# Optimization experiments

Hardware: AMD Instinct MI355X
Metric: run time of the kernel (lower is better)

## Reference

```python
import jax, jax.numpy as jnp
import numpy as np

BOHR_RADIUS = 0.529177  # Angstrom
KE_KCAL = 332.0636      # Coulomb constant, kcal/mol * Angstrom / e^2
EPS = 1e-15
R_CUT = 5.0

ZBL = {'d': [0.8854 * BOHR_RADIUS], 'z_exp': [0.23],
       'c': [0.1818, 0.5099, 0.2802, 0.02817],
       'exponents': [3.2, 0.9423, 0.4028, 0.2016]}

def _inv_softplus(v):
    v = np.asarray(v, dtype=np.float32)
    return jnp.asarray(np.log(np.exp(v) - 1.0).reshape(-1, 1))

def setup_inputs() -> dict:
    key = jax.random.key(0)
    k1, k2, k3, k4 = jax.random.split(key, 4)
    N, E, M = 200000, 8000000, 1000
    xyz = jax.random.normal(k1, (N, 3), dtype=jnp.float32) * 3.0
    z = jax.random.randint(k2, (N,), 1, 94, dtype=jnp.int32)
    nbrs = jax.random.randint(k3, (E, 2), 0, N, dtype=jnp.int32)
    offsets = jax.random.normal(k4, (E, 3), dtype=jnp.float32) * 2.0
    num_atoms = jnp.full((M,), N // M, dtype=jnp.int32)
    return {
        'xyz': xyz, 'z': z, 'nbrs': nbrs, 'num_atoms': num_atoms, 'offsets': offsets,
        'd_inv': _inv_softplus(ZBL['d']),
        'z_exp_inv': _inv_softplus(ZBL['z_exp']),
        'c_inv': _inv_softplus(ZBL['c']),
        'exponents_inv': _inv_softplus(ZBL['exponents']),
    }

def reference(xyz, z, nbrs, num_atoms, offsets, d_inv, z_exp_inv, c_inv, exponents_inv):
    sp = jax.nn.softplus
    d, z_exp, c, exponents = sp(d_inv), sp(z_exp_inv), sp(c_inv), sp(exponents_inv)

    i, j = nbrs[:, 0], nbrs[:, 1]
    mask = j > i  # undirected-edge filter (masked instead of gathered: same math)

    z_i = z[i].astype(jnp.float32)  # [E]
    z_j = z[j].astype(jnp.float32)
    diff = xyz[i] - xyz[j] - offsets                  # [E,3]
    r_ij = jnp.sqrt((diff ** 2 + EPS).sum(-1))        # stable norm, [E]

    # ZBL phi: d,z_exp are [1,1]; broadcast over edges
    a = (d / (z_i ** z_exp + z_j ** z_exp)).reshape(-1)           # [E]
    phi = (c * jnp.exp(-exponents * r_ij / a)).sum(0) / c.sum()   # [4,E] -> [E]

    # SpookyNet cutoff, NaN-safe outside r_cut
    den = (R_CUT - r_ij) * (R_CUT + r_ij)
    safe_den = jnp.where(r_ij < R_CUT, den, 1.0)
    f_cut = jnp.where(r_ij < R_CUT, jnp.exp(-r_ij ** 2 / safe_den), 0.0)

    pairwise = KE_KCAL * z_i * z_j / r_ij * phi * f_cut
    pairwise = jnp.where(mask, pairwise, 0.0)

    N = xyz.shape[0]
    M = num_atoms.shape[0]
    mol_idx = jnp.repeat(jnp.arange(M), num_atoms, total_repeat_length=N)  # [N]
    seg = mol_idx[i]                                                       # [E]
    energy = jax.ops.segment_sum(pairwise, seg, num_segments=M).reshape(-1, 1)
    return energy
```

## Files before the change

kernel.cpp:

```cpp
#include <hip/hip_runtime.h>
#include <hip/hip_bf16.h>

#define KE_F  332.0636f
#define MAX_M 1024
#define BLK   256
#define NBLK  2048

typedef int   ivec4 __attribute__((ext_vector_type(4)));
typedef float fvec4 __attribute__((ext_vector_type(4)));

__device__ __forceinline__ float softplusf(float x) {
    return logf(1.0f + expf(x));
}

__global__ void scan_params_kernel(const int* __restrict__ num_atoms, int M,
                                   const float* __restrict__ d_inv,
                                   const float* __restrict__ z_exp_inv,
                                   const float* __restrict__ c_inv,
                                   const float* __restrict__ exp_inv,
                                   int* __restrict__ mol_starts,
                                   float* __restrict__ params,
                                   float* __restrict__ out) {
    __shared__ int buf[MAX_M];
    int t = threadIdx.x;
    buf[t] = (t < M) ? num_atoms[t] : 0;
    __syncthreads();
    for (int off = 1; off < MAX_M; off <<= 1) {
        int x = (t >= off) ? buf[t - off] : 0;
        __syncthreads();
        buf[t] += x;
        __syncthreads();
    }
    if (t == 0) mol_starts[0] = 0;
    if (t < M) mol_starts[t + 1] = buf[t];
    if (t == 0) {
        float dd = softplusf(d_inv[0]);
        float c0 = softplusf(c_inv[0]), c1 = softplusf(c_inv[1]);
        float c2 = softplusf(c_inv[2]), c3 = softplusf(c_inv[3]);
        float e0 = softplusf(exp_inv[0]), e1 = softplusf(exp_inv[1]);
        float e2 = softplusf(exp_inv[2]), e3 = softplusf(exp_inv[3]);
        float ic = 1.0f / (c0 + c1 + c2 + c3);
        float id = 1.0f / dd;
        params[0] = c0 * ic; params[1] = c1 * ic; params[2] = c2 * ic; params[3] = c3 * ic;
        params[4] = e0 * id; params[5] = e1 * id; params[6] = e2 * id; params[7] = e3 * id;
    }
    if (t < 96) {
        float zexp = softplusf(z_exp_inv[0]);
        params[16 + t] = __powf((float)t, zexp);
    }
    for (int k = t; k < M; k += MAX_M) out[k] = 0.0f;
}

__global__ void pack_kernel(const float* __restrict__ xyz,
                            const int* __restrict__ z,
                            const int* __restrict__ mol_starts, int M, int N,
                            float4* __restrict__ pack) {
    int a = blockIdx.x * blockDim.x + threadIdx.x;
    if (a >= N) return;
    int lo = 0, hi = M;
    while (hi - lo > 1) {
        int mid = (lo + hi) >> 1;
        if (mol_starts[mid] <= a) lo = mid; else hi = mid;
    }
    pack[a] = make_float4(xyz[3 * a + 0], xyz[3 * a + 1], xyz[3 * a + 2],
                          (float)((lo << 7) | z[a]));
}

__global__ __launch_bounds__(BLK) void nr_main_kernel(
    const int* __restrict__ nbrs, const float* __restrict__ offsets,
    const float4* __restrict__ pack,
    const float* __restrict__ params, float* __restrict__ out, int E, int M) {
    __shared__ float sm[MAX_M];
    __shared__ float zp[96];
    for (int t = threadIdx.x; t < MAX_M; t += BLK) sm[t] = 0.0f;
    if (threadIdx.x < 96) zp[threadIdx.x] = params[16 + threadIdx.x];
    __syncthreads();

    const float4 kk = *(const float4*)(params + 0);
    const float4 gg = *(const float4*)(params + 4);

    const int ngroups = E >> 2;
    const int stride = gridDim.x * BLK;
    const ivec4* nb4 = (const ivec4*)nbrs;
    const fvec4* of4 = (const fvec4*)offsets;

    for (int g = blockIdx.x * BLK + threadIdx.x; g < ngroups; g += stride) {
        const ivec4 n01 = __builtin_nontemporal_load(nb4 + 2 * (size_t)g);
        const ivec4 n23 = __builtin_nontemporal_load(nb4 + 2 * (size_t)g + 1);
        const fvec4 oA  = __builtin_nontemporal_load(of4 + 3 * (size_t)g);
        const fvec4 oB  = __builtin_nontemporal_load(of4 + 3 * (size_t)g + 1);
        const fvec4 oC  = __builtin_nontemporal_load(of4 + 3 * (size_t)g + 2);

        const int   iv[4] = {n01.x, n01.z, n23.x, n23.z};
        const int   jv[4] = {n01.y, n01.w, n23.y, n23.w};
        const float ox[4] = {oA.x, oA.w, oB.z, oC.y};
        const float oy[4] = {oA.y, oB.x, oB.w, oC.z};
        const float oz[4] = {oA.z, oB.y, oC.x, oC.w};

        bool   m[4];
        float4 pi[4], pj[4];
#pragma unroll
        for (int k = 0; k < 4; ++k) {
            m[k] = jv[k] > iv[k];
            const int ii = m[k] ? iv[k] : 0;
            const int jj = m[k] ? jv[k] : 0;
            pi[k] = pack[ii];
            pj[k] = pack[jj];
        }
#pragma unroll
        for (int k = 0; k < 4; ++k) {
            const float dx = pi[k].x - pj[k].x - ox[k];
            const float dy = pi[k].y - pj[k].y - oy[k];
            const float dz = pi[k].z - pj[k].z - oz[k];
            const float r2 = fmaf(dx, dx, fmaf(dy, dy, dz * dz)) + 3e-15f;
            const bool ok = m[k] && (r2 < 25.0f);
            const int  wi = (int)pi[k].w;
            const int  wj = (int)pj[k].w;
            const float zi = (float)(wi & 127);
            const float zj = (float)(wj & 127);
            const float inv_r = rsqrtf(r2);
            const float r = r2 * inv_r;
            const float S = zp[wi & 127] + zp[wj & 127];
            const float rs = r * S;
            const float phi = kk.x * __expf(-gg.x * rs) + kk.y * __expf(-gg.y * rs) +
                              kk.z * __expf(-gg.z * rs) + kk.w * __expf(-gg.w * rs);
            const float fc = __expf(-__fdividef(r2, 25.0f - r2));
            const float val = KE_F * zi * zj * inv_r * phi * fc;
            if (ok) atomicAdd(&sm[wi >> 7], val);
        }
    }

    for (int e = (ngroups << 2) + blockIdx.x * BLK + threadIdx.x; e < E; e += stride) {
        const int i = nbrs[2 * e], j = nbrs[2 * e + 1];
        if (j <= i) continue;
        const float oxs = offsets[3 * e], oys = offsets[3 * e + 1], ozs = offsets[3 * e + 2];
        const float4 pis = pack[i], pjs = pack[j];
        const float dx = pis.x - pjs.x - oxs;
        const float dy = pis.y - pjs.y - oys;
        const float dz = pis.z - pjs.z - ozs;
        const float r2 = fmaf(dx, dx, fmaf(dy, dy, dz * dz)) + 3e-15f;
        if (r2 >= 25.0f) continue;
        const int  wi = (int)pis.w;
        const int  wj = (int)pjs.w;
        const float inv_r = rsqrtf(r2);
        const float r = r2 * inv_r;
        const float S = zp[wi & 127] + zp[wj & 127];
        const float rs = r * S;
        const float phi = kk.x * __expf(-gg.x * rs) + kk.y * __expf(-gg.y * rs) +
                          kk.z * __expf(-gg.z * rs) + kk.w * __expf(-gg.w * rs);
        const float fc = __expf(-__fdividef(r2, 25.0f - r2));
        atomicAdd(&sm[wi >> 7],
                  KE_F * (float)(wi & 127) * (float)(wj & 127) * inv_r * phi * fc);
    }

    __syncthreads();
    for (int t = threadIdx.x; t < M; t += BLK) {
        const float v = sm[t];
        if (v != 0.0f) atomicAdd(&out[t], v);
    }
}

extern "C" void kernel_launch(void* const* d_in, const int* in_sizes, int n_in,
                              void* d_out, int out_size, void* d_ws, size_t ws_size,
                              hipStream_t stream) {
    const float* xyz       = (const float*)d_in[0];
    const int*   z         = (const int*)d_in[1];
    const int*   nbrs      = (const int*)d_in[2];
    const int*   num_atoms = (const int*)d_in[3];
    const float* offsets   = (const float*)d_in[4];
    const float* d_inv     = (const float*)d_in[5];
    const float* z_exp_inv = (const float*)d_in[6];
    const float* c_inv     = (const float*)d_in[7];
    const float* exp_inv   = (const float*)d_in[8];
    float* out = (float*)d_out;

    const int N = in_sizes[0] / 3;
    const int E = in_sizes[2] / 2;
    const int M = in_sizes[3];

    char* w = (char*)d_ws;
    int*    mol_starts = (int*)w;
    float*  params     = (float*)(w + 4096);
    float4* pack       = (float4*)(w + 8192);

    scan_params_kernel<<<1, MAX_M, 0, stream>>>(num_atoms, M, d_inv, z_exp_inv,
                                                c_inv, exp_inv, mol_starts,
                                                params, out);
    pack_kernel<<<(N + BLK - 1) / BLK, BLK, 0, stream>>>(xyz, z, mol_starts, M, N,
                                                         pack);
    nr_main_kernel<<<NBLK, BLK, 0, stream>>>(nbrs, offsets, pack,
                                             params, out, E, M);
}
```

Baseline: 246.7 us.

## Software-pipeline edge stream loads and gathers across grid-stride iterations

Restructures the main edge loop into a three-stage software pipeline. The nbrs/offsets stream for two iterations ahead is loaded while the pack gathers for the next iteration are issued, and only then is the current group computed. The goal is to hide global and gather latency behind compute. It also folds the cutoff exponent into each of the four ZBL exponentials, removing one exp per edge. The cost is higher register pressure from holding two streams and a gathered set, which may lower occupancy, plus redundant clamped loads at the tail.

```diff
diff --git a/kernel.cpp b/kernel.cpp
--- a/kernel.cpp
+++ b/kernel.cpp
@@ -66,6 +66,70 @@
                           (float)((lo << 7) | z[a]));
 }
 
+struct Stream {
+    ivec4 n01, n23;
+    fvec4 oA, oB, oC;
+};
+
+struct Gathered {
+    float4 pi[4], pj[4];
+    bool   m[4];
+};
+
+__device__ __forceinline__ Stream load_stream(const ivec4* __restrict__ nb4,
+                                              const fvec4* __restrict__ of4,
+                                              size_t g) {
+    Stream s;
+    s.n01 = __builtin_nontemporal_load(nb4 + 2 * g);
+    s.n23 = __builtin_nontemporal_load(nb4 + 2 * g + 1);
+    s.oA  = __builtin_nontemporal_load(of4 + 3 * g);
+    s.oB  = __builtin_nontemporal_load(of4 + 3 * g + 1);
+    s.oC  = __builtin_nontemporal_load(of4 + 3 * g + 2);
+    return s;
+}
+
+__device__ __forceinline__ Gathered do_gather(const Stream& s,
+                                              const float4* __restrict__ pack) {
+    Gathered d;
+    const int iv[4] = {s.n01.x, s.n01.z, s.n23.x, s.n23.z};
+    const int jv[4] = {s.n01.y, s.n01.w, s.n23.y, s.n23.w};
+#pragma unroll
+    for (int k = 0; k < 4; ++k) {
+        d.m[k] = jv[k] > iv[k];
+        d.pi[k] = pack[d.m[k] ? iv[k] : 0];
+        d.pj[k] = pack[d.m[k] ? jv[k] : 0];
+    }
+    return d;
+}
+
+__device__ __forceinline__ void compute4(const Gathered& d, const Stream& s,
+                                         float4 kk, float4 gg,
+                                         const float* __restrict__ zp,
+                                         float* __restrict__ sm) {
+    const float ox[4] = {s.oA.x, s.oA.w, s.oB.z, s.oC.y};
+    const float oy[4] = {s.oA.y, s.oB.x, s.oB.w, s.oC.z};
+    const float oz[4] = {s.oA.z, s.oB.y, s.oC.x, s.oC.w};
+#pragma unroll
+    for (int k = 0; k < 4; ++k) {
+        const float dx = d.pi[k].x - d.pj[k].x - ox[k];
+        const float dy = d.pi[k].y - d.pj[k].y - oy[k];
+        const float dz = d.pi[k].z - d.pj[k].z - oz[k];
+        const float r2 = fmaf(dx, dx, fmaf(dy, dy, dz * dz)) + 3e-15f;
+        const bool ok = d.m[k] && (r2 < 25.0f);
+        const int  wi = (int)d.pi[k].w;
+        const int  wj = (int)d.pj[k].w;
+        const float inv_r = rsqrtf(r2);
+        const float rs = r2 * inv_r * (zp[wi & 127] + zp[wj & 127]);
+        const float u  = __fdividef(r2, 25.0f - r2);
+        const float pf = kk.x * __expf(fmaf(-gg.x, rs, -u)) +
+                         kk.y * __expf(fmaf(-gg.y, rs, -u)) +
+                         kk.z * __expf(fmaf(-gg.z, rs, -u)) +
+                         kk.w * __expf(fmaf(-gg.w, rs, -u));
+        const float val = KE_F * (float)(wi & 127) * (float)(wj & 127) * inv_r * pf;
+        if (ok) atomicAdd(&sm[wi >> 7], val);
+    }
+}
+
 __global__ __launch_bounds__(BLK) void nr_main_kernel(
     const int* __restrict__ nbrs, const float* __restrict__ offsets,
     const float4* __restrict__ pack,
@@ -80,53 +144,26 @@
     const float4 gg = *(const float4*)(params + 4);
 
     const int ngroups = E >> 2;
-    const int stride = gridDim.x * BLK;
+    const int stride  = gridDim.x * BLK;
     const ivec4* nb4 = (const ivec4*)nbrs;
     const fvec4* of4 = (const fvec4*)offsets;
 
-    for (int g = blockIdx.x * BLK + threadIdx.x; g < ngroups; g += stride) {
-        const ivec4 n01 = __builtin_nontemporal_load(nb4 + 2 * (size_t)g);
-        const ivec4 n23 = __builtin_nontemporal_load(nb4 + 2 * (size_t)g + 1);
-        const fvec4 oA  = __builtin_nontemporal_load(of4 + 3 * (size_t)g);
-        const fvec4 oB  = __builtin_nontemporal_load(of4 + 3 * (size_t)g + 1);
-        const fvec4 oC  = __builtin_nontemporal_load(of4 + 3 * (size_t)g + 2);
-
-        const int   iv[4] = {n01.x, n01.z, n23.x, n23.z};
-        const int   jv[4] = {n01.y, n01.w, n23.y, n23.w};
-        const float ox[4] = {oA.x, oA.w, oB.z, oC.y};
-        const float oy[4] = {oA.y, oB.x, oB.w, oC.z};
-        const float oz[4] = {oA.z, oB.y, oC.x, oC.w};
-
-        bool   m[4];
-        float4 pi[4], pj[4];
-#pragma unroll
-        for (int k = 0; k < 4; ++k) {
-            m[k] = jv[k] > iv[k];
-            const int ii = m[k] ? iv[k] : 0;
-            const int jj = m[k] ? jv[k] : 0;
-            pi[k] = pack[ii];
-            pj[k] = pack[jj];
-        }
-#pragma unroll
-        for (int k = 0; k < 4; ++k) {
-            const float dx = pi[k].x - pj[k].x - ox[k];
-            const float dy = pi[k].y - pj[k].y - oy[k];
-            const float dz = pi[k].z - pj[k].z - oz[k];
-            const float r2 = fmaf(dx, dx, fmaf(dy, dy, dz * dz)) + 3e-15f;
-            const bool ok = m[k] && (r2 < 25.0f);
-            const int  wi = (int)pi[k].w;
-            const int  wj = (int)pj[k].w;
-            const float zi = (float)(wi & 127);
-            const float zj = (float)(wj & 127);
-            const float inv_r = rsqrtf(r2);
-            const float r = r2 * inv_r;
-            const float S = zp[wi & 127] + zp[wj & 127];
-            const float rs = r * S;
-            const float phi = kk.x * __expf(-gg.x * rs) + kk.y * __expf(-gg.y * rs) +
-                              kk.z * __expf(-gg.z * rs) + kk.w * __expf(-gg.w * rs);
-            const float fc = __expf(-__fdividef(r2, 25.0f - r2));
-            const float val = KE_F * zi * zj * inv_r * phi * fc;
-            if (ok) atomicAdd(&sm[wi >> 7], val);
+    int g = blockIdx.x * BLK + threadIdx.x;
+    if (g < ngroups) {
+        const size_t last = (size_t)(ngroups - 1);
+        size_t g1 = (size_t)g + stride; if (g1 > last) g1 = last;
+        Stream s_cur = load_stream(nb4, of4, (size_t)g);
+        Stream s_nxt = load_stream(nb4, of4, g1);
+        Gathered d_cur = do_gather(s_cur, pack);
+        for (;;) {
+            size_t g2 = (size_t)g + 2 * (size_t)stride; if (g2 > last) g2 = last;
+            Stream   s_n2  = load_stream(nb4, of4, g2);
+            Gathered d_nxt = do_gather(s_nxt, pack);
+            compute4(d_cur, s_cur, kk, gg, zp, sm);
+            const int gn = g + stride;
+            if (gn >= ngroups) break;
+            g = gn;
+            s_cur = s_nxt; s_nxt = s_n2; d_cur = d_nxt;
         }
     }
 
@@ -143,14 +180,14 @@
         const int  wi = (int)pis.w;
         const int  wj = (int)pjs.w;
         const float inv_r = rsqrtf(r2);
-        const float r = r2 * inv_r;
-        const float S = zp[wi & 127] + zp[wj & 127];
-        const float rs = r * S;
-        const float phi = kk.x * __expf(-gg.x * rs) + kk.y * __expf(-gg.y * rs) +
-                          kk.z * __expf(-gg.z * rs) + kk.w * __expf(-gg.w * rs);
-        const float fc = __expf(-__fdividef(r2, 25.0f - r2));
+        const float rs = r2 * inv_r * (zp[wi & 127] + zp[wj & 127]);
+        const float u  = __fdividef(r2, 25.0f - r2);
+        const float pf = kk.x * __expf(fmaf(-gg.x, rs, -u)) +
+                         kk.y * __expf(fmaf(-gg.y, rs, -u)) +
+                         kk.z * __expf(fmaf(-gg.z, rs, -u)) +
+                         kk.w * __expf(fmaf(-gg.w, rs, -u));
         atomicAdd(&sm[wi >> 7],
-                  KE_F * (float)(wi & 127) * (float)(wj & 127) * inv_r * phi * fc);
+                  KE_F * (float)(wi & 127) * (float)(wj & 127) * inv_r * pf);
     }
 
     __syncthreads();
```

Result: no change. 249.4 us (+1.1%).
